# Performance work log

Hardware: AMD Instinct MI355X
Metric: run time of the kernel (lower is better)

Reference implementation:

```python
import jax, jax.numpy as jnp
import numpy as np

B = 4096
C3 = 1.0 / np.sqrt(3.0)
# Wigner 3j tensors for the l<=1 paths (e3nn real basis)
W3J_000 = jnp.ones((1, 1, 1), dtype=jnp.float32)
W3J_110 = (jnp.eye(3) * C3).reshape(3, 3, 1).astype(jnp.float32)
W3J_011 = (jnp.eye(3) * C3).reshape(1, 3, 3).astype(jnp.float32)
W3J_101 = (jnp.eye(3) * C3).reshape(3, 1, 3).astype(jnp.float32)


def setup_inputs() -> dict:
    key = jax.random.key(0)
    ks = jax.random.split(key, 10)
    n = lambda k, s: jax.random.normal(k, s, dtype=jnp.float32)
    return {
        "feat": n(ks[0], (B, 320)),        # 128x0e + 64x1o
        "node_emb": n(ks[1], (B, 128)),
        # o3.Linear(irreps_node -> irreps_block): one mixing matrix per l
        "W0": n(ks[2], (128, 16)),          # 0e: 128 -> 16
        "W1": n(ks[3], (64, 16)),           # 1o: 64 -> 16
        # lin_weight MLP: 128 -> 64 -> 36864
        "lw1": n(ks[4], (128, 64)) * 0.1, "lb1": jnp.zeros((64,), jnp.float32),
        "lw2": n(ks[5], (64, 36864)) * 0.1, "lb2": jnp.zeros((36864,), jnp.float32),
        # lin_bias MLP: 128 -> 64 -> 1280
        "bw1": n(ks[6], (128, 64)) * 0.1, "bb1": jnp.zeros((64,), jnp.float32),
        "bw2": n(ks[7], (64, 1280)) * 0.1, "bb2": jnp.zeros((1280,), jnp.float32),
    }


def _path(x, wpath, w3j, bias):
    # x: [B, mul_in, dim_in]; wpath: [B, mul_in, u, v]; w3j: [i, j, k]
    r = jnp.einsum('bwuv,bwk->buvk', wpath, x)
    if bias is not None:
        r = r + bias[..., None]
    out = jnp.einsum('ijk,buvk->buivj', w3j, r) / x.shape[1]
    b, u, i, v, j = out.shape
    return out.reshape(b, u * i, v * j)


def reference(feat, node_emb, W0, W1, lw1, lb1, lw2, lb2, bw1, bb1, bw2, bb2):
    bn = feat.shape[0]
    # split feat into irreps: 128x0e | 64x1o
    s = feat[:, :128].reshape(bn, 128, 1)
    v = feat[:, 128:].reshape(bn, 64, 3)
    # o3.Linear with e3nn path normalization 1/sqrt(fan_in)
    x0 = jnp.einsum('buk,uv->bvk', s, W0) / np.sqrt(128.0)  # [B,16,1]
    x1 = jnp.einsum('buk,uv->bvk', v, W1) / np.sqrt(64.0)   # [B,16,3]
    # per-sample path weights and biases
    w = jax.nn.silu(node_emb @ lw1 + lb1) @ lw2 + lb2        # [B,36864]
    bb = jax.nn.silu(node_emb @ bw1 + bb1) @ bw2 + bb2       # [B,1280]
    # weight slices per instruction (flat layout matches instruction order)
    w00 = w[:, :16384].reshape(bn, 16, 32, 32)               # 0e -> (0e,0e)
    w11 = w[:, 16384:20480].reshape(bn, 16, 16, 16)          # 0e -> (1o,1o)
    w01 = w[:, 20480:28672].reshape(bn, 16, 32, 16)          # 1o -> (0e,1o)
    w10 = w[:, 28672:36864].reshape(bn, 16, 16, 32)          # 1o -> (1o,0e)
    b00 = bb[:, :1024].reshape(bn, 32, 32)
    b11 = bb[:, 1024:1280].reshape(bn, 16, 16)
    blk00 = _path(x0, w00, W3J_000, b00)   # [B,32,32]
    blk11 = _path(x0, w11, W3J_110, b11)   # [B,48,48]
    blk01 = _path(x1, w01, W3J_011, None)  # [B,32,48]
    blk10 = _path(x1, w10, W3J_101, None)  # [B,48,32]
    top = jnp.concatenate([blk00, blk01], axis=-1)
    bot = jnp.concatenate([blk10, blk11], axis=-1)
    return jnp.concatenate([top, bot], axis=-2)  # [B,80,80]
```

## Files before the change

### kernel.cpp

```cpp
#include <hip/hip_runtime.h>
#include <hip/hip_bf16.h>
#include <math.h>


typedef short bf16x8 __attribute__((ext_vector_type(8)));
typedef float f32x4 __attribute__((ext_vector_type(4)));

static __device__ __forceinline__ short f2bf(float f) {
  unsigned u = __builtin_bit_cast(unsigned, f);
  u = u + 0x7fffu + ((u >> 16) & 1u);
  return (short)(u >> 16);
}

__global__ void k_transpose(const float* __restrict__ lw2, short* __restrict__ lw2f) {
  __shared__ float tile[64][65];
  int n0 = blockIdx.x * 64;
  int t = threadIdx.x;
#pragma unroll
  for (int k = 0; k < 16; ++k) {
    int idx = k * 256 + t;
    int c = idx >> 6, j = idx & 63;
    tile[c][j] = lw2[(size_t)c * 36864 + n0 + j];
  }
  __syncthreads();
#pragma unroll
  for (int k = 0; k < 16; ++k) {
    int idx = k * 256 + t;
    int e = idx & 7, l = (idx >> 3) & 63, half = (idx >> 9) & 1, nbl = idx >> 10;
    int q = l >> 4, colr = l & 15;
    int j = nbl * 16 + colr;
    int c = half * 32 + q * 8 + e;
    size_t nb = (size_t)(n0 >> 4) + nbl;
    lw2f[((nb * 2 + half) * 64 + l) * 8 + e] = f2bf(tile[c][j]);
  }
}

__global__ void k_bias(const float* __restrict__ bw2, const float* __restrict__ lb2,
                       const float* __restrict__ bb2,
                       short* __restrict__ bbf00, short* __restrict__ bbf11,
                       short* __restrict__ bbf01, short* __restrict__ bbf10) {
  int i = blockIdx.x * 256 + threadIdx.x;
  if (i < 98304) {
    int uvb = i / 1536, r = i % 1536;
    int kk = r >> 9, l = (r >> 3) & 63, e = r & 7;
    int q = l >> 4, col = l & 15;
    int uv = uvb * 16 + col, k = kk * 32 + q * 8 + e;
    float v = 0.0f;
    if (k < 64) v = bw2[k * 1280 + uv];
    else if (k < 80) v = lb2[(k - 64) * 1024 + uv];
    else if (k == 80) v = bb2[uv];
    bbf00[i] = f2bf(v);
  } else if (i < 122880) {
    int j = i - 98304;
    int uvb = j / 1536, r = j % 1536;
    int kk = r >> 9, l = (r >> 3) & 63, e = r & 7;
    int q = l >> 4, col = l & 15;
    int uv = uvb * 16 + col, k = kk * 32 + q * 8 + e;
    float v = 0.0f;
    if (k < 64) v = bw2[k * 1280 + 1024 + uv];
    else if (k < 80) v = lb2[16384 + (k - 64) * 256 + uv];
    else if (k == 80) v = bb2[1024 + uv];
    bbf11[j] = f2bf(v);
  } else if (i < 139264) {
    int j = i - 122880;
    int uvb = j >> 9, r = j & 511;
    int l = (r >> 3) & 63, e = r & 7;
    int q = l >> 4, col = l & 15;
    int uv = uvb * 16 + col, k = q * 8 + e;
    bbf01[j] = (k < 16) ? f2bf(lb2[20480 + k * 512 + uv]) : (short)0;
  } else if (i < 155648) {
    int j = i - 139264;
    int uvb = j >> 9, r = j & 511;
    int l = (r >> 3) & 63, e = r & 7;
    int q = l >> 4, col = l & 15;
    int uv = uvb * 16 + col, k = q * 8 + e;
    bbf10[j] = (k < 16) ? f2bf(lb2[28672 + k * 512 + uv]) : (short)0;
  }
}

__global__ void k_samples(const float* __restrict__ feat, const float* __restrict__ ne,
                          const float* __restrict__ W0, const float* __restrict__ W1,
                          const float* __restrict__ lw1, const float* __restrict__ lb1,
                          const float* __restrict__ bw1, const float* __restrict__ bb1,
                          float* __restrict__ H, float* __restrict__ H2,
                          float* __restrict__ X0, float* __restrict__ X1) {
  int b = blockIdx.x;
  int t = threadIdx.x;
  __shared__ float sne[128];
  __shared__ float sf[320];
  if (t < 128) sne[t] = ne[(size_t)b * 128 + t];
  for (int i = t; i < 320; i += 192) sf[i] = feat[(size_t)b * 320 + i];
  __syncthreads();
  if (t < 64) {
    float a = lb1[t];
    for (int k = 0; k < 128; ++k) a += sne[k] * lw1[k * 64 + t];
    H[(size_t)b * 64 + t] = a / (1.0f + expf(-a));
  } else if (t < 128) {
    int c = t - 64;
    float a = bb1[c];
    for (int k = 0; k < 128; ++k) a += sne[k] * bw1[k * 64 + c];
    H2[(size_t)b * 64 + c] = a / (1.0f + expf(-a));
  } else if (t < 144) {
    int v = t - 128;
    float a = 0.0f;
    for (int u = 0; u < 128; ++u) a += sf[u] * W0[u * 16 + v];
    X0[(size_t)b * 16 + v] = a * 0.08838834764831845f;
  } else {
    int idx = t - 144, v = idx / 3, j = idx % 3;
    float a = 0.0f;
    for (int u = 0; u < 64; ++u) a += sf[128 + u * 3 + j] * W1[u * 16 + v];
    X1[(size_t)b * 48 + v * 3 + j] = a * 0.125f;
  }
}

template <int N, int NB16, int NS16, int NBIAS>
static __device__ __forceinline__ void mmA2(
    const short* __restrict__ LW2F, const short* __restrict__ BBF,
    const short* __restrict__ sQp, const short* __restrict__ sAbp,
    int uvb, int lane, f32x4 (&acc)[2][N]) {
  const int lane8 = lane * 8;
  auto bptr = [&](int kk, int i) -> const bf16x8* {
    return (const bf16x8*)(LW2F +
        ((size_t)(NB16 + (kk >> 1) * NS16 + uvb + i) * 2 + (kk & 1)) * 512 + lane8);
  };
  bf16x8 B[4][N];
#pragma unroll
  for (int d = 0; d < 4; ++d)
#pragma unroll
    for (int i = 0; i < N; ++i) B[d][i] = *bptr(d, i);
#pragma unroll
  for (int kk = 0; kk < 32; ++kk) {
    const int d = kk & 3;
    const bf16x8 A0 = *(const bf16x8*)(sQp + kk * 512 + lane8);
    const bf16x8 A1 = *(const bf16x8*)(sQp + 16384 + kk * 512 + lane8);
#pragma unroll
    for (int i = 0; i < N; ++i) {
      acc[0][i] = __builtin_amdgcn_mfma_f32_16x16x32_bf16(A0, B[d][i], acc[0][i], 0, 0, 0);
      acc[1][i] = __builtin_amdgcn_mfma_f32_16x16x32_bf16(A1, B[d][i], acc[1][i], 0, 0, 0);
    }
    if (kk + 4 < 32) {
#pragma unroll
      for (int i = 0; i < N; ++i) B[d][i] = *bptr(kk + 4, i);
    }
  }
#pragma unroll
  for (int kk = 0; kk < NBIAS; ++kk) {
    const bf16x8 Ab0 = *(const bf16x8*)(sAbp + kk * 512 + lane8);
    const bf16x8 Ab1 = *(const bf16x8*)(sAbp + NBIAS * 512 + kk * 512 + lane8);
#pragma unroll
    for (int i = 0; i < N; ++i) {
      const bf16x8 Bx = *(const bf16x8*)(BBF +
          (size_t)((uvb + i) * NBIAS + kk) * 512 + lane8);
      acc[0][i] = __builtin_amdgcn_mfma_f32_16x16x32_bf16(Ab0, Bx, acc[0][i], 0, 0, 0);
      acc[1][i] = __builtin_amdgcn_mfma_f32_16x16x32_bf16(Ab1, Bx, acc[1][i], 0, 0, 0);
    }
  }
}

template <int NP, int N, int NB16, int NS16>
static __device__ __forceinline__ void mmBnp(
    const short* __restrict__ LW2F, const short* __restrict__ BBF,
    const short* __restrict__ sQp, const short* __restrict__ sA1p,
    int uvb, int lane, f32x4 (&acc)[NP][N]) {
  const int lane8 = lane * 8;
  auto bptr = [&](int kk, int i) -> const bf16x8* {
    return (const bf16x8*)(LW2F +
        ((size_t)(NB16 + (kk >> 1) * NS16 + uvb + i) * 2 + (kk & 1)) * 512 + lane8);
  };
  bf16x8 B[4][N];
#pragma unroll
  for (int d = 0; d < 4; ++d)
#pragma unroll
    for (int i = 0; i < N; ++i) B[d][i] = *bptr(d, i);
#pragma unroll
  for (int kk = 0; kk < 32; ++kk) {
    const int d = kk & 3;
    bf16x8 A[NP];
#pragma unroll
    for (int p = 0; p < NP; ++p)
      A[p] = *(const bf16x8*)(sQp + p * 16384 + kk * 512 + lane8);
#pragma unroll
    for (int i = 0; i < N; ++i)
#pragma unroll
      for (int p = 0; p < NP; ++p)
        acc[p][i] = __builtin_amdgcn_mfma_f32_16x16x32_bf16(A[p], B[d][i], acc[p][i], 0, 0, 0);
    if (kk + 4 < 32) {
#pragma unroll
      for (int i = 0; i < N; ++i) B[d][i] = *bptr(kk + 4, i);
    }
  }
#pragma unroll
  for (int i = 0; i < N; ++i) {
    const bf16x8 Bx = *(const bf16x8*)(BBF + (size_t)(uvb + i) * 512 + lane8);
#pragma unroll
    for (int p = 0; p < NP; ++p) {
      const bf16x8 Ap = *(const bf16x8*)(sA1p + p * 512 + lane8);
      acc[p][i] = __builtin_amdgcn_mfma_f32_16x16x32_bf16(Ap, Bx, acc[p][i], 0, 0, 0);
    }
  }
}

__global__ __launch_bounds__(512, 1) void k_main(
    const short* __restrict__ LW2F,
    const short* __restrict__ BBF00, const short* __restrict__ BBF11,
    const short* __restrict__ BBF01, const short* __restrict__ BBF10,
    const float* __restrict__ H, const float* __restrict__ H2,
    const float* __restrict__ X0, const float* __restrict__ X1,
    float* __restrict__ out) {
  constexpr float S00 = 0.0625f;
  constexpr float S3 = 0.036084391824351614f;

  int idx = blockIdx.x;
  int slot = idx & 7;
  int h = slot >> 2;
  int s = (slot & 3) + 4 * (idx >> 3);
  int b0 = s << 5;
  int t = threadIdx.x;
  int lane = t & 63, wave = t >> 6;
  int col = lane & 15, q = lane >> 4;

  __shared__ float sH[32][66];
  __shared__ float sX0[32][17];
  __shared__ float sX1[32][51];
  __shared__ short sQ[4][32][4][16][8];
  __shared__ short sAb[2][3][4][16][8];
  __shared__ short sA1[3][2][4][16][8];

  for (int i = t; i < 2048; i += 512)
    sH[i >> 6][i & 63] = H[(size_t)(b0 + (i >> 6)) * 64 + (i & 63)];
  sX0[t >> 4][t & 15] = X0[(size_t)(b0 + (t >> 4)) * 16 + (t & 15)];
  for (int i = t; i < 1536; i += 512)
    sX1[i / 48][i % 48] = X1[(size_t)(b0 + i / 48) * 48 + (i % 48)];
  __syncthreads();

  for (int i = t; i < 16384; i += 512) {
    int p = i >> 13, rem = i & 8191;
    int kk = rem >> 8, qq = (rem >> 6) & 3, cc = (rem >> 2) & 15, e2 = (rem & 3) << 1;
    int k = kk * 32 + qq * 8 + e2;
    int w = k >> 6, c = k & 63;
    float xw = sX0[p * 16 + cc][w];
    unsigned lo = (unsigned short)f2bf(sH[p * 16 + cc][c] * xw);
    unsigned hi = (unsigned short)f2bf(sH[p * 16 + cc][c + 1] * xw);
    *(unsigned*)&sQ[p][kk][qq][cc][e2] = lo | (hi << 16);
  }
  for (int i = t; i < 3072; i += 512) {
    int g = (i >= 1536), rem = i - (g ? 1536 : 0);
    int kk = rem >> 9, r2 = rem & 511;
    int qq = r2 >> 7, cc = (r2 >> 3) & 15, e = r2 & 7;
    int k = kk * 32 + qq * 8 + e;
    float v = 0.0f;
    if (k < 64) v = H2[(size_t)(b0 + g * 16 + cc) * 64 + k];
    else if (k < 80) v = sX0[g * 16 + cc][k - 64];
    else if (k == 80) v = 1.0f;
    sAb[g][kk][qq][cc][e] = f2bf(v);
  }
  for (int i = t; i < 3072; i += 512) {
    int j = i >> 10, rem = i & 1023;
    int g = rem >> 9, r2 = rem & 511;
    int qq = r2 >> 7, cc = (r2 >> 3) & 15, e = r2 & 7;
    int k = qq * 8 + e;
    sA1[j][g][qq][cc][e] = (k < 16) ? f2bf(sX1[g * 16 + cc][k * 3 + j]) : (short)0;
  }
  __syncthreads();

  {
    int uvb = h * 32 + wave * 4;
    f32x4 acc[2][4] = {};
    mmA2<4, 0, 64, 3>(LW2F, BBF00, &sQ[0][0][0][0][0], &sAb[0][0][0][0][0],
                      uvb, lane, acc);
#pragma unroll
    for (int g = 0; g < 2; ++g)
#pragma unroll
      for (int i = 0; i < 4; ++i)
#pragma unroll
        for (int ii = 0; ii < 4; ++ii) {
          size_t ob = (size_t)(b0 + g * 16 + q * 4 + ii) * 6400;
          int uv = (uvb + i) * 16 + col;
          out[ob + (uv >> 5) * 80 + (uv & 31)] = acc[g][i][ii] * S00;
        }
  }
  {
    int uvb = h * 8 + wave;
    f32x4 acc[2][1] = {};
    mmA2<1, 1024, 16, 3>(LW2F, BBF11, &sQ[0][0][0][0][0], &sAb[0][0][0][0][0],
                         uvb, lane, acc);
#pragma unroll
    for (int g = 0; g < 2; ++g)
#pragma unroll
      for (int ii = 0; ii < 4; ++ii) {
        size_t ob = (size_t)(b0 + g * 16 + q * 4 + ii) * 6400;
        int uv = uvb * 16 + col;
        float val = acc[g][0][ii] * S3;
        int u = uv >> 4, v = uv & 15;
        float* p = out + ob + (size_t)(32 + 3 * u) * 80 + (32 + 3 * v);
        p[0] = val;   p[1] = 0.f;   p[2] = 0.f;
        p[80] = 0.f;  p[81] = val;  p[82] = 0.f;
        p[160] = 0.f; p[161] = 0.f; p[162] = val;
      }
  }

  __syncthreads();
  for (int i = t; i < 32768; i += 512) {
    int p = i >> 13, rem = i & 8191;
    int j = p >> 1, g = p & 1;
    int kk = rem >> 8, qq = (rem >> 6) & 3, cc = (rem >> 2) & 15, e2 = (rem & 3) << 1;
    int k = kk * 32 + qq * 8 + e2;
    int w = k >> 6, c = k & 63;
    float xw = sX1[g * 16 + cc][w * 3 + j];
    unsigned lo = (unsigned short)f2bf(sH[g * 16 + cc][c] * xw);
    unsigned hi = (unsigned short)f2bf(sH[g * 16 + cc][c + 1] * xw);
    *(unsigned*)&sQ[p][kk][qq][cc][e2] = lo | (hi << 16);
  }
  __syncthreads();
  {
    int uvb = h * 16 + wave * 2;
    {
      f32x4 acc[4][2] = {};
      mmBnp<4, 2, 1280, 32>(LW2F, BBF01, &sQ[0][0][0][0][0],
                            &sA1[0][0][0][0][0], uvb, lane, acc);
#pragma unroll
      for (int p = 0; p < 4; ++p)
#pragma unroll
        for (int i = 0; i < 2; ++i)
#pragma unroll
          for (int ii = 0; ii < 4; ++ii) {
            int j = p >> 1, g = p & 1;
            size_t ob = (size_t)(b0 + g * 16 + q * 4 + ii) * 6400;
            int uv = (uvb + i) * 16 + col;
            out[ob + (uv >> 4) * 80 + 32 + 3 * (uv & 15) + j] = acc[p][i][ii] * S3;
          }
    }
    {
      f32x4 acc[4][2] = {};
      mmBnp<4, 2, 1792, 32>(LW2F, BBF10, &sQ[0][0][0][0][0],
                            &sA1[0][0][0][0][0], uvb, lane, acc);
#pragma unroll
      for (int p = 0; p < 4; ++p)
#pragma unroll
        for (int i = 0; i < 2; ++i)
#pragma unroll
          for (int ii = 0; ii < 4; ++ii) {
            int j = p >> 1, g = p & 1;
            size_t ob = (size_t)(b0 + g * 16 + q * 4 + ii) * 6400;
            int uv = (uvb + i) * 16 + col;
            out[ob + (size_t)(32 + 3 * (uv >> 5) + j) * 80 + (uv & 31)] = acc[p][i][ii] * S3;
          }
    }
  }

  __syncthreads();
  for (int i = t; i < 16384; i += 512) {
    int g = i >> 13, rem = i & 8191;
    int kk = rem >> 8, qq = (rem >> 6) & 3, cc = (rem >> 2) & 15, e2 = (rem & 3) << 1;
    int k = kk * 32 + qq * 8 + e2;
    int w = k >> 6, c = k & 63;
    float xw = sX1[g * 16 + cc][w * 3 + 2];
    unsigned lo = (unsigned short)f2bf(sH[g * 16 + cc][c] * xw);
    unsigned hi = (unsigned short)f2bf(sH[g * 16 + cc][c + 1] * xw);
    *(unsigned*)&sQ[g][kk][qq][cc][e2] = lo | (hi << 16);
  }
  __syncthreads();
  {
    int uvb = h * 16 + wave * 2;
    {
      f32x4 acc[2][2] = {};
      mmBnp<2, 2, 1280, 32>(LW2F, BBF01, &sQ[0][0][0][0][0],
                            &sA1[2][0][0][0][0], uvb, lane, acc);
#pragma unroll
      for (int g = 0; g < 2; ++g)
#pragma unroll
        for (int i = 0; i < 2; ++i)
#pragma unroll
          for (int ii = 0; ii < 4; ++ii) {
            size_t ob = (size_t)(b0 + g * 16 + q * 4 + ii) * 6400;
            int uv = (uvb + i) * 16 + col;
            out[ob + (uv >> 4) * 80 + 32 + 3 * (uv & 15) + 2] = acc[g][i][ii] * S3;
          }
    }
    {
      f32x4 acc[2][2] = {};
      mmBnp<2, 2, 1792, 32>(LW2F, BBF10, &sQ[0][0][0][0][0],
                            &sA1[2][0][0][0][0], uvb, lane, acc);
#pragma unroll
      for (int g = 0; g < 2; ++g)
#pragma unroll
        for (int i = 0; i < 2; ++i)
#pragma unroll
          for (int ii = 0; ii < 4; ++ii) {
            size_t ob = (size_t)(b0 + g * 16 + q * 4 + ii) * 6400;
            int uv = (uvb + i) * 16 + col;
            out[ob + (size_t)(32 + 3 * (uv >> 5) + 2) * 80 + (uv & 31)] = acc[g][i][ii] * S3;
          }
    }
  }
}

extern "C" void kernel_launch(void* const* d_in, const int* in_sizes, int n_in,
                              void* d_out, int out_size, void* d_ws, size_t ws_size,
                              hipStream_t stream) {
  const float* feat = (const float*)d_in[0];
  const float* ne   = (const float*)d_in[1];
  const float* W0   = (const float*)d_in[2];
  const float* W1   = (const float*)d_in[3];
  const float* lw1  = (const float*)d_in[4];
  const float* lb1  = (const float*)d_in[5];
  const float* lw2  = (const float*)d_in[6];
  const float* lb2  = (const float*)d_in[7];
  const float* bw1  = (const float*)d_in[8];
  const float* bb1  = (const float*)d_in[9];
  const float* bw2  = (const float*)d_in[10];
  const float* bb2  = (const float*)d_in[11];

  char* ws = (char*)d_ws;
  short* LW2F = (short*)ws; ws += (size_t)36864 * 64 * 2;
  short* BBF00 = (short*)ws; ws += (size_t)98304 * 2;
  short* BBF11 = (short*)ws; ws += (size_t)24576 * 2;
  short* BBF01 = (short*)ws; ws += (size_t)16384 * 2;
  short* BBF10 = (short*)ws; ws += (size_t)16384 * 2;
  float* H  = (float*)ws;   ws += (size_t)4096 * 64 * 4;
  float* H2 = (float*)ws;   ws += (size_t)4096 * 64 * 4;
  float* X0 = (float*)ws;   ws += (size_t)4096 * 16 * 4;
  float* X1 = (float*)ws;   ws += (size_t)4096 * 48 * 4;
  (void)ws_size; (void)in_sizes; (void)n_in; (void)out_size;

  hipLaunchKernelGGL(k_transpose, dim3(576), dim3(256), 0, stream, lw2, LW2F);
  hipLaunchKernelGGL(k_bias, dim3(608), dim3(256), 0, stream, bw2, lb2, bb2,
                     BBF00, BBF11, BBF01, BBF10);
  hipLaunchKernelGGL(k_samples, dim3(4096), dim3(192), 0, stream,
                     feat, ne, W0, W1, lw1, lb1, bw1, bb1, H, H2, X0, X1);
  hipLaunchKernelGGL(k_main, dim3(256), dim3(512), 0, stream,
                     LW2F, BBF00, BBF11, BBF01, BBF10, H, H2, X0, X1, (float*)d_out);
}
```

Baseline: 138.3 us.

## Precompute bf16 operand tiles in separate kernel and double waves in main kernel

```diff
diff --git a/kernel.cpp b/kernel.cpp
--- a/kernel.cpp
+++ b/kernel.cpp
@@ -113,165 +113,154 @@
   }
 }
 
-template <int N, int NB16, int NS16, int NBIAS>
-static __device__ __forceinline__ void mmA2(
-    const short* __restrict__ LW2F, const short* __restrict__ BBF,
-    const short* __restrict__ sQp, const short* __restrict__ sAbp,
-    int uvb, int lane, f32x4 (&acc)[2][N]) {
-  const int lane8 = lane * 8;
+__global__ void k_q(const float* __restrict__ H, const float* __restrict__ H2,
+                    const float* __restrict__ X0, const float* __restrict__ X1,
+                    short* __restrict__ QF, short* __restrict__ AbF,
+                    short* __restrict__ A1F) {
+  int g16 = blockIdx.x;
+  int b0 = g16 * 16;
+  int t = threadIdx.x;
+  __shared__ float sH[16][64];
+  __shared__ float sH2[16][64];
+  __shared__ float sX0[16][16];
+  __shared__ float sX1[16][48];
+  for (int i = t; i < 1024; i += 256) {
+    sH [i >> 6][i & 63] = H [(size_t)(b0 + (i >> 6)) * 64 + (i & 63)];
+    sH2[i >> 6][i & 63] = H2[(size_t)(b0 + (i >> 6)) * 64 + (i & 63)];
+  }
+  sX0[t >> 4][t & 15] = X0[(size_t)(b0 + (t >> 4)) * 16 + (t & 15)];
+  for (int i = t; i < 768; i += 256)
+    sX1[i / 48][i % 48] = X1[(size_t)(b0 + i / 48) * 48 + (i % 48)];
+  __syncthreads();
+  for (int i = t; i < 32768; i += 256) {
+    int p = i >> 13, rem = i & 8191;
+    int kk = rem >> 8, lane = (rem >> 2) & 63, e2 = (rem & 3) << 1;
+    int cc = lane & 15, q = lane >> 4;
+    int k = kk * 32 + q * 8 + e2;
+    int w = k >> 6, c = k & 63;
+    float xw = (p == 0) ? sX0[cc][w] : sX1[cc][w * 3 + (p - 1)];
+    unsigned lo = (unsigned short)f2bf(sH[cc][c] * xw);
+    unsigned hi = (unsigned short)f2bf(sH[cc][c + 1] * xw);
+    ((unsigned*)QF)[(size_t)g16 * 32768 + i] = lo | (hi << 16);
+  }
+  for (int i = t; i < 1536; i += 256) {
+    int kk = i >> 9, lane = (i >> 3) & 63, e = i & 7;
+    int cc = lane & 15, q = lane >> 4;
+    int k = kk * 32 + q * 8 + e;
+    float v = 0.0f;
+    if (k < 64) v = sH2[cc][k];
+    else if (k < 80) v = sX0[cc][k - 64];
+    else if (k == 80) v = 1.0f;
+    AbF[(size_t)g16 * 1536 + i] = f2bf(v);
+  }
+  for (int i = t; i < 1536; i += 256) {
+    int j = i >> 9, r = i & 511;
+    int lane = r >> 3, e = r & 7;
+    int cc = lane & 15, q = lane >> 4;
+    int k = q * 8 + e;
+    A1F[(size_t)g16 * 1536 + i] = (k < 16) ? f2bf(sX1[cc][k * 3 + j]) : (short)0;
+  }
+}
+
+template <int NP, int N, int NB16, int NS16>
+static __device__ __forceinline__ void mm_stream(
+    const short* __restrict__ LW2F, const short* __restrict__ sQ0,
+    int uvb, int lane8, f32x4 (&acc)[NP][N]) {
   auto bptr = [&](int kk, int i) -> const bf16x8* {
     return (const bf16x8*)(LW2F +
         ((size_t)(NB16 + (kk >> 1) * NS16 + uvb + i) * 2 + (kk & 1)) * 512 + lane8);
   };
-  bf16x8 B[4][N];
-#pragma unroll
-  for (int d = 0; d < 4; ++d)
+  bf16x8 B[2][N];
+#pragma unroll
+  for (int d = 0; d < 2; ++d)
 #pragma unroll
     for (int i = 0; i < N; ++i) B[d][i] = *bptr(d, i);
 #pragma unroll
   for (int kk = 0; kk < 32; ++kk) {
-    const int d = kk & 3;
-    const bf16x8 A0 = *(const bf16x8*)(sQp + kk * 512 + lane8);
-    const bf16x8 A1 = *(const bf16x8*)(sQp + 16384 + kk * 512 + lane8);
-#pragma unroll
-    for (int i = 0; i < N; ++i) {
-      acc[0][i] = __builtin_amdgcn_mfma_f32_16x16x32_bf16(A0, B[d][i], acc[0][i], 0, 0, 0);
-      acc[1][i] = __builtin_amdgcn_mfma_f32_16x16x32_bf16(A1, B[d][i], acc[1][i], 0, 0, 0);
-    }
-    if (kk + 4 < 32) {
-#pragma unroll
-      for (int i = 0; i < N; ++i) B[d][i] = *bptr(kk + 4, i);
-    }
-  }
-#pragma unroll
-  for (int kk = 0; kk < NBIAS; ++kk) {
-    const bf16x8 Ab0 = *(const bf16x8*)(sAbp + kk * 512 + lane8);
-    const bf16x8 Ab1 = *(const bf16x8*)(sAbp + NBIAS * 512 + kk * 512 + lane8);
-#pragma unroll
-    for (int i = 0; i < N; ++i) {
-      const bf16x8 Bx = *(const bf16x8*)(BBF +
-          (size_t)((uvb + i) * NBIAS + kk) * 512 + lane8);
-      acc[0][i] = __builtin_amdgcn_mfma_f32_16x16x32_bf16(Ab0, Bx, acc[0][i], 0, 0, 0);
-      acc[1][i] = __builtin_amdgcn_mfma_f32_16x16x32_bf16(Ab1, Bx, acc[1][i], 0, 0, 0);
-    }
-  }
-}
-
-template <int NP, int N, int NB16, int NS16>
-static __device__ __forceinline__ void mmBnp(
-    const short* __restrict__ LW2F, const short* __restrict__ BBF,
-    const short* __restrict__ sQp, const short* __restrict__ sA1p,
-    int uvb, int lane, f32x4 (&acc)[NP][N]) {
-  const int lane8 = lane * 8;
-  auto bptr = [&](int kk, int i) -> const bf16x8* {
-    return (const bf16x8*)(LW2F +
-        ((size_t)(NB16 + (kk >> 1) * NS16 + uvb + i) * 2 + (kk & 1)) * 512 + lane8);
-  };
-  bf16x8 B[4][N];
-#pragma unroll
-  for (int d = 0; d < 4; ++d)
-#pragma unroll
-    for (int i = 0; i < N; ++i) B[d][i] = *bptr(d, i);
-#pragma unroll
-  for (int kk = 0; kk < 32; ++kk) {
-    const int d = kk & 3;
+    const int d = kk & 1;
     bf16x8 A[NP];
 #pragma unroll
     for (int p = 0; p < NP; ++p)
-      A[p] = *(const bf16x8*)(sQp + p * 16384 + kk * 512 + lane8);
+      A[p] = *(const bf16x8*)(sQ0 + p * 16384 + kk * 512 + lane8);
 #pragma unroll
     for (int i = 0; i < N; ++i)
 #pragma unroll
       for (int p = 0; p < NP; ++p)
         acc[p][i] = __builtin_amdgcn_mfma_f32_16x16x32_bf16(A[p], B[d][i], acc[p][i], 0, 0, 0);
-    if (kk + 4 < 32) {
-#pragma unroll
-      for (int i = 0; i < N; ++i) B[d][i] = *bptr(kk + 4, i);
-    }
-  }
-#pragma unroll
-  for (int i = 0; i < N; ++i) {
-    const bf16x8 Bx = *(const bf16x8*)(BBF + (size_t)(uvb + i) * 512 + lane8);
-#pragma unroll
-    for (int p = 0; p < NP; ++p) {
-      const bf16x8 Ap = *(const bf16x8*)(sA1p + p * 512 + lane8);
-      acc[p][i] = __builtin_amdgcn_mfma_f32_16x16x32_bf16(Ap, Bx, acc[p][i], 0, 0, 0);
-    }
-  }
-}
-
-__global__ __launch_bounds__(512, 1) void k_main(
+    if (kk + 2 < 32) {
+#pragma unroll
+      for (int i = 0; i < N; ++i) B[d][i] = *bptr(kk + 2, i);
+    }
+  }
+}
+
+template <int NP, int N, int NBIAS>
+static __device__ __forceinline__ void mm_bias(
+    const short* __restrict__ BBF, const short* __restrict__ Ab0, int astride,
+    int uvb, int lane8, f32x4 (&acc)[NP][N]) {
+#pragma unroll
+  for (int kk = 0; kk < NBIAS; ++kk)
+#pragma unroll
+    for (int i = 0; i < N; ++i) {
+      const bf16x8 Bx = *(const bf16x8*)(BBF + (size_t)((uvb + i) * NBIAS + kk) * 512 + lane8);
+#pragma unroll
+      for (int p = 0; p < NP; ++p) {
+        const bf16x8 Ap = *(const bf16x8*)(Ab0 + p * astride + kk * 512 + lane8);
+        acc[p][i] = __builtin_amdgcn_mfma_f32_16x16x32_bf16(Ap, Bx, acc[p][i], 0, 0, 0);
+      }
+    }
+}
+
+__global__ __launch_bounds__(1024, 1) void k_main(
     const short* __restrict__ LW2F,
     const short* __restrict__ BBF00, const short* __restrict__ BBF11,
     const short* __restrict__ BBF01, const short* __restrict__ BBF10,
-    const float* __restrict__ H, const float* __restrict__ H2,
-    const float* __restrict__ X0, const float* __restrict__ X1,
-    float* __restrict__ out) {
+    const short* __restrict__ QF, const short* __restrict__ AbF,
+    const short* __restrict__ A1F, float* __restrict__ out) {
   constexpr float S00 = 0.0625f;
   constexpr float S3 = 0.036084391824351614f;
 
-  int idx = blockIdx.x;
-  int slot = idx & 7;
-  int h = slot >> 2;
-  int s = (slot & 3) + 4 * (idx >> 3);
+  int bidx = blockIdx.x;
+  int xslot = bidx & 7;
+  int h = xslot >> 2;
+  int s = (xslot & 3) + 4 * (bidx >> 3);
   int b0 = s << 5;
   int t = threadIdx.x;
-  int lane = t & 63, wave = t >> 6;
+  int lane = t & 63, slot = t >> 6;
   int col = lane & 15, q = lane >> 4;
-
-  __shared__ float sH[32][66];
-  __shared__ float sX0[32][17];
-  __shared__ float sX1[32][51];
-  __shared__ short sQ[4][32][4][16][8];
-  __shared__ short sAb[2][3][4][16][8];
-  __shared__ short sA1[3][2][4][16][8];
-
-  for (int i = t; i < 2048; i += 512)
-    sH[i >> 6][i & 63] = H[(size_t)(b0 + (i >> 6)) * 64 + (i & 63)];
-  sX0[t >> 4][t & 15] = X0[(size_t)(b0 + (t >> 4)) * 16 + (t & 15)];
-  for (int i = t; i < 1536; i += 512)
-    sX1[i / 48][i % 48] = X1[(size_t)(b0 + i / 48) * 48 + (i % 48)];
-  __syncthreads();
-
-  for (int i = t; i < 16384; i += 512) {
-    int p = i >> 13, rem = i & 8191;
-    int kk = rem >> 8, qq = (rem >> 6) & 3, cc = (rem >> 2) & 15, e2 = (rem & 3) << 1;
-    int k = kk * 32 + qq * 8 + e2;
-    int w = k >> 6, c = k & 63;
-    float xw = sX0[p * 16 + cc][w];
-    unsigned lo = (unsigned short)f2bf(sH[p * 16 + cc][c] * xw);
-    unsigned hi = (unsigned short)f2bf(sH[p * 16 + cc][c + 1] * xw);
-    *(unsigned*)&sQ[p][kk][qq][cc][e2] = lo | (hi << 16);
-  }
-  for (int i = t; i < 3072; i += 512) {
-    int g = (i >= 1536), rem = i - (g ? 1536 : 0);
-    int kk = rem >> 9, r2 = rem & 511;
-    int qq = r2 >> 7, cc = (r2 >> 3) & 15, e = r2 & 7;
-    int k = kk * 32 + qq * 8 + e;
-    float v = 0.0f;
-    if (k < 64) v = H2[(size_t)(b0 + g * 16 + cc) * 64 + k];
-    else if (k < 80) v = sX0[g * 16 + cc][k - 64];
-    else if (k == 80) v = 1.0f;
-    sAb[g][kk][qq][cc][e] = f2bf(v);
-  }
-  for (int i = t; i < 3072; i += 512) {
-    int j = i >> 10, rem = i & 1023;
-    int g = rem >> 9, r2 = rem & 511;
-    int qq = r2 >> 7, cc = (r2 >> 3) & 15, e = r2 & 7;
-    int k = qq * 8 + e;
-    sA1[j][g][qq][cc][e] = (k < 16) ? f2bf(sX1[g * 16 + cc][k * 3 + j]) : (short)0;
+  int lane8 = lane * 8;
+
+  __shared__ short sQ[4 * 16384];
+  __shared__ short sAb[2 * 1536];
+  __shared__ short sA1[6 * 512];
+
+  for (int i = t; i < 384; i += 1024) {
+    int g = i >= 192, r = i - g * 192;
+    ((uint4*)(sAb + g * 1536))[r] =
+        ((const uint4*)(AbF + (size_t)(s * 2 + g) * 1536))[r];
+  }
+  for (int i = t; i < 384; i += 1024) {
+    int jp = i >> 6, r = i & 63;
+    int j = jp >> 1, g = jp & 1;
+    ((uint4*)(sA1 + jp * 512))[r] =
+        ((const uint4*)(A1F + ((size_t)(s * 2 + g) * 3 + j) * 512))[r];
+  }
+  for (int i = t; i < 4096; i += 1024) {
+    int pl = i >> 11, r = i & 2047;
+    const uint4* src = (const uint4*)(QF + (size_t)(s * 2 + pl) * 65536);
+    ((uint4*)sQ)[pl * 2048 + r] = src[r];
   }
   __syncthreads();
 
   {
-    int uvb = h * 32 + wave * 4;
-    f32x4 acc[2][4] = {};
-    mmA2<4, 0, 64, 3>(LW2F, BBF00, &sQ[0][0][0][0][0], &sAb[0][0][0][0][0],
-                      uvb, lane, acc);
+    int uvb = h * 32 + slot * 2;
+    f32x4 acc[2][2] = {};
+    mm_stream<2, 2, 0, 64>(LW2F, sQ, uvb, lane8, acc);
+    mm_bias<2, 2, 3>(BBF00, sAb, 1536, uvb, lane8, acc);
 #pragma unroll
     for (int g = 0; g < 2; ++g)
 #pragma unroll
-      for (int i = 0; i < 4; ++i)
+      for (int i = 0; i < 2; ++i)
 #pragma unroll
         for (int ii = 0; ii < 4; ++ii) {
           size_t ob = (size_t)(b0 + g * 16 + q * 4 + ii) * 6400;
@@ -279,11 +268,11 @@
           out[ob + (uv >> 5) * 80 + (uv & 31)] = acc[g][i][ii] * S00;
         }
   }
-  {
-    int uvb = h * 8 + wave;
+  if (slot < 8) {
+    int uvb = h * 8 + slot;
     f32x4 acc[2][1] = {};
-    mmA2<1, 1024, 16, 3>(LW2F, BBF11, &sQ[0][0][0][0][0], &sAb[0][0][0][0][0],
-                         uvb, lane, acc);
+    mm_stream<2, 1, 1024, 16>(LW2F, sQ, uvb, lane8, acc);
+    mm_bias<2, 1, 3>(BBF11, sAb, 1536, uvb, lane8, acc);
 #pragma unroll
     for (int g = 0; g < 2; ++g)
 #pragma unroll
@@ -300,97 +289,79 @@
   }
 
   __syncthreads();
-  for (int i = t; i < 32768; i += 512) {
-    int p = i >> 13, rem = i & 8191;
-    int j = p >> 1, g = p & 1;
-    int kk = rem >> 8, qq = (rem >> 6) & 3, cc = (rem >> 2) & 15, e2 = (rem & 3) << 1;
-    int k = kk * 32 + qq * 8 + e2;
-    int w = k >> 6, c = k & 63;
-    float xw = sX1[g * 16 + cc][w * 3 + j];
-    unsigned lo = (unsigned short)f2bf(sH[g * 16 + cc][c] * xw);
-    unsigned hi = (unsigned short)f2bf(sH[g * 16 + cc][c + 1] * xw);
-    *(unsigned*)&sQ[p][kk][qq][cc][e2] = lo | (hi << 16);
+  for (int i = t; i < 8192; i += 1024) {
+    int pl = i >> 11, r = i & 2047;
+    const uint4* src = (const uint4*)(QF +
+        ((size_t)(s * 2 + (pl & 1)) * 4 + 1 + (pl >> 1)) * 16384);
+    ((uint4*)sQ)[pl * 2048 + r] = src[r];
   }
   __syncthreads();
   {
-    int uvb = h * 16 + wave * 2;
+    int uvb = h * 16 + slot;
     {
-      f32x4 acc[4][2] = {};
-      mmBnp<4, 2, 1280, 32>(LW2F, BBF01, &sQ[0][0][0][0][0],
-                            &sA1[0][0][0][0][0], uvb, lane, acc);
+      f32x4 acc[4][1] = {};
+      mm_stream<4, 1, 1280, 32>(LW2F, sQ, uvb, lane8, acc);
+      mm_bias<4, 1, 1>(BBF01, sA1, 512, uvb, lane8, acc);
 #pragma unroll
       for (int p = 0; p < 4; ++p)
 #pragma unroll
-        for (int i = 0; i < 2; ++i)
-#pragma unroll
-          for (int ii = 0; ii < 4; ++ii) {
-            int j = p >> 1, g = p & 1;
-            size_t ob = (size_t)(b0 + g * 16 + q * 4 + ii) * 6400;
-            int uv = (uvb + i) * 16 + col;
-            out[ob + (uv >> 4) * 80 + 32 + 3 * (uv & 15) + j] = acc[p][i][ii] * S3;
-          }
+        for (int ii = 0; ii < 4; ++ii) {
+          int j = p >> 1, g = p & 1;
+          size_t ob = (size_t)(b0 + g * 16 + q * 4 + ii) * 6400;
+          int uv = uvb * 16 + col;
+          out[ob + (uv >> 4) * 80 + 32 + 3 * (uv & 15) + j] = acc[p][0][ii] * S3;
+        }
     }
     {
-      f32x4 acc[4][2] = {};
-      mmBnp<4, 2, 1792, 32>(LW2F, BBF10, &sQ[0][0][0][0][0],
-                            &sA1[0][0][0][0][0], uvb, lane, acc);
+      f32x4 acc[4][1] = {};
+      mm_stream<4, 1, 1792, 32>(LW2F, sQ, uvb, lane8, acc);
+      mm_bias<4, 1, 1>(BBF10, sA1, 512, uvb, lane8, acc);
 #pragma unroll
       for (int p = 0; p < 4; ++p)
 #pragma unroll
-        for (int i = 0; i < 2; ++i)
-#pragma unroll
-          for (int ii = 0; ii < 4; ++ii) {
-            int j = p >> 1, g = p & 1;
-            size_t ob = (size_t)(b0 + g * 16 + q * 4 + ii) * 6400;
-            int uv = (uvb + i) * 16 + col;
-            out[ob + (size_t)(32 + 3 * (uv >> 5) + j) * 80 + (uv & 31)] = acc[p][i][ii] * S3;
-          }
-    }
-  }
-
-  __syncthreads();
-  for (int i = t; i < 16384; i += 512) {
-    int g = i >> 13, rem = i & 8191;
-    int kk = rem >> 8, qq = (rem >> 6) & 3, cc = (rem >> 2) & 15, e2 = (rem & 3) << 1;
-    int k = kk * 32 + qq * 8 + e2;
-    int w = k >> 6, c = k & 63;
-    float xw = sX1[g * 16 + cc][w * 3 + 2];
-    unsigned lo = (unsigned short)f2bf(sH[g * 16 + cc][c] * xw);
-    unsigned hi = (unsigned short)f2bf(sH[g * 16 + cc][c + 1] * xw);
-    *(unsigned*)&sQ[g][kk][qq][cc][e2] = lo | (hi << 16);
+        for (int ii = 0; ii < 4; ++ii) {
+          int j = p >> 1, g = p & 1;
+          size_t ob = (size_t)(b0 + g * 16 + q * 4 + ii) * 6400;
+          int uv = uvb * 16 + col;
+          out[ob + (size_t)(32 + 3 * (uv >> 5) + j) * 80 + (uv & 31)] = acc[p][0][ii] * S3;
+        }
+    }
+  }
+
+  __syncthreads();
+  for (int i = t; i < 4096; i += 1024) {
+    int pl = i >> 11, r = i & 2047;
+    const uint4* src = (const uint4*)(QF + ((size_t)(s * 2 + pl) * 4 + 3) * 16384);
+    ((uint4*)sQ)[pl * 2048 + r] = src[r];
   }
   __syncthreads();
   {
-    int uvb = h * 16 + wave * 2;
+    int uvb = h * 16 + slot;
     {
-      f32x4 acc[2][2] = {};
-      mmBnp<2, 2, 1280, 32>(LW2F, BBF01, &sQ[0][0][0][0][0],
-                            &sA1[2][0][0][0][0], uvb, lane, acc);
+      f32x4 acc[2][1] = {};
+      mm_stream<2, 1, 1280, 32>(LW2F, sQ, uvb, lane8, acc);
+      mm_bias<2, 1, 1>(BBF01, sA1 + 4 * 512, 512, uvb, lane8, acc);
 #pragma unroll
       for (int g = 0; g < 2; ++g)
 #pragma unroll
-        for (int i = 0; i < 2; ++i)
-#pragma unroll
-          for (int ii = 0; ii < 4; ++ii) {
-            size_t ob = (size_t)(b0 + g * 16 + q * 4 + ii) * 6400;
-            int uv = (uvb + i) * 16 + col;
-            out[ob + (uv >> 4) * 80 + 32 + 3 * (uv & 15) + 2] = acc[g][i][ii] * S3;
-          }
+        for (int ii = 0; ii < 4; ++ii) {
+          size_t ob = (size_t)(b0 + g * 16 + q * 4 + ii) * 6400;
+          int uv = uvb * 16 + col;
+          out[ob + (uv >> 4) * 80 + 32 + 3 * (uv & 15) + 2] = acc[g][0][ii] * S3;
+        }
     }
     {
-      f32x4 acc[2][2] = {};
-      mmBnp<2, 2, 1792, 32>(LW2F, BBF10, &sQ[0][0][0][0][0],
-                            &sA1[2][0][0][0][0], uvb, lane, acc);
+      f32x4 acc[2][1] = {};
+      mm_stream<2, 1, 1792, 32>(LW2F, sQ, uvb, lane8, acc);
+      mm_bias<2, 1, 1>(BBF10, sA1 + 4 * 512, 512, uvb, lane8, acc);
 #pragma unroll
       for (int g = 0; g < 2; ++g)
 #pragma unroll
-        for (int i = 0; i < 2; ++i)
-#pragma unroll
-          for (int ii = 0; ii < 4; ++ii) {
-            size_t ob = (size_t)(b0 + g * 16 + q * 4 + ii) * 6400;
-            int uv = (uvb + i) * 16 + col;
-            out[ob + (size_t)(32 + 3 * (uv >> 5) + 2) * 80 + (uv & 31)] = acc[g][i][ii] * S3;
-          }
+        for (int ii = 0; ii < 4; ++ii) {
+          size_t ob = (size_t)(b0 + g * 16 + q * 4 + ii) * 6400;
+          int uv = uvb * 16 + col;
+          out[ob + (size_t)(32 + 3 * (uv >> 5) + 2) * 80 + (uv & 31)] = acc[g][0][ii] * S3;
+        }
     }
   }
 }
@@ -412,7 +383,7 @@
   const float* bb2  = (const float*)d_in[11];
 
   char* ws = (char*)d_ws;
-  short* LW2F = (short*)ws; ws += (size_t)36864 * 64 * 2;
+  short* LW2F  = (short*)ws; ws += (size_t)36864 * 64 * 2;
   short* BBF00 = (short*)ws; ws += (size_t)98304 * 2;
   short* BBF11 = (short*)ws; ws += (size_t)24576 * 2;
   short* BBF01 = (short*)ws; ws += (size_t)16384 * 2;
@@ -421,6 +392,9 @@
   float* H2 = (float*)ws;   ws += (size_t)4096 * 64 * 4;
   float* X0 = (float*)ws;   ws += (size_t)4096 * 16 * 4;
   float* X1 = (float*)ws;   ws += (size_t)4096 * 48 * 4;
+  short* QF  = (short*)ws;  ws += (size_t)256 * 65536 * 2;
+  short* AbF = (short*)ws;  ws += (size_t)256 * 1536 * 2;
+  short* A1F = (short*)ws;  ws += (size_t)256 * 1536 * 2;
   (void)ws_size; (void)in_sizes; (void)n_in; (void)out_size;
 
   hipLaunchKernelGGL(k_transpose, dim3(576), dim3(256), 0, stream, lw2, LW2F);
@@ -428,6 +402,8 @@
                      BBF00, BBF11, BBF01, BBF10);
   hipLaunchKernelGGL(k_samples, dim3(4096), dim3(192), 0, stream,
                      feat, ne, W0, W1, lw1, lb1, bw1, bb1, H, H2, X0, X1);
-  hipLaunchKernelGGL(k_main, dim3(256), dim3(512), 0, stream,
-                     LW2F, BBF00, BBF11, BBF01, BBF10, H, H2, X0, X1, (float*)d_out);
-}
+  hipLaunchKernelGGL(k_q, dim3(256), dim3(256), 0, stream,
+                     H, H2, X0, X1, QF, AbF, A1F);
+  hipLaunchKernelGGL(k_main, dim3(256), dim3(1024), 0, stream,
+                     LW2F, BBF00, BBF11, BBF01, BBF10, QF, AbF, A1F, (float*)d_out);
+}
```

Result: slower. 151.5 us (+9.6%).
